# Kernel tuning notes

Hardware: AMD Instinct MI355X
Metric: run time of the kernel (lower is better)

Reference implementation:

```python
import jax, jax.numpy as jnp
import numpy as np

N_EMBED, D = 200000, 128
B, K = 50000, 32


def setup_inputs() -> dict:
    key = jax.random.key(0)
    k1, k2, k3 = jax.random.split(key, 3)
    embedding = jax.random.normal(k1, (N_EMBED, D), dtype=jnp.float32)
    self_feats = jax.random.normal(k2, (B, D), dtype=jnp.float32)
    neighbor_idx = jax.random.randint(k3, (B, K), 0, N_EMBED, dtype=jnp.int32)
    return {"embedding": embedding, "self_feats": self_feats, "neighbor_idx": neighbor_idx}


def reference(embedding, self_feats, neighbor_idx):
    # Original builds a row-normalized 0/1 mask over unique neighbors and does
    # mask @ embed_matrix == per-node mean of neighbor embeddings.
    neigh = jnp.take(embedding, neighbor_idx, axis=0)   # [B, K, D] gather
    feats_1 = jnp.mean(neigh, axis=1)                   # [B, D] segment-mean
    feats_2 = self_feats - feats_1                      # [B, D]
    return jnp.concatenate((feats_1, feats_2), axis=1)  # [B, 2D]
```

## Files before the change

### kernel.cpp

```cpp
#include <hip/hip_runtime.h>


constexpr int D = 128;
constexpr int K = 32;
constexpr int ROW_WORDS = D / 4;

typedef float f32x2 __attribute__((ext_vector_type(2)));

__global__ __launch_bounds__(256) void convert_f32_to_fp8(
    const float* __restrict__ in, unsigned int* __restrict__ out, int n16)
{
    int i = blockIdx.x * blockDim.x + threadIdx.x;
    if (i >= n16) return;
    const float4* p = reinterpret_cast<const float4*>(in) + (size_t)i * 4;
    float4 a = p[0], b = p[1], c = p[2], d = p[3];
    unsigned int w0 = 0, w1 = 0, w2 = 0, w3 = 0;
    w0 = __builtin_amdgcn_cvt_pk_fp8_f32(a.x, a.y, w0, false);
    w0 = __builtin_amdgcn_cvt_pk_fp8_f32(a.z, a.w, w0, true);
    w1 = __builtin_amdgcn_cvt_pk_fp8_f32(b.x, b.y, w1, false);
    w1 = __builtin_amdgcn_cvt_pk_fp8_f32(b.z, b.w, w1, true);
    w2 = __builtin_amdgcn_cvt_pk_fp8_f32(c.x, c.y, w2, false);
    w2 = __builtin_amdgcn_cvt_pk_fp8_f32(c.z, c.w, w2, true);
    w3 = __builtin_amdgcn_cvt_pk_fp8_f32(d.x, d.y, w3, false);
    w3 = __builtin_amdgcn_cvt_pk_fp8_f32(d.z, d.w, w3, true);
    uint4 pack; pack.x = w0; pack.y = w1; pack.z = w2; pack.w = w3;
    reinterpret_cast<uint4*>(out)[i] = pack;
}

__device__ __forceinline__ void acc_fp8x16(float* acc, const uint4& e)
{
    f32x2 t;
    t = __builtin_amdgcn_cvt_pk_f32_fp8(e.x, false); acc[0]  += t.x; acc[1]  += t.y;
    t = __builtin_amdgcn_cvt_pk_f32_fp8(e.x, true ); acc[2]  += t.x; acc[3]  += t.y;
    t = __builtin_amdgcn_cvt_pk_f32_fp8(e.y, false); acc[4]  += t.x; acc[5]  += t.y;
    t = __builtin_amdgcn_cvt_pk_f32_fp8(e.y, true ); acc[6]  += t.x; acc[7]  += t.y;
    t = __builtin_amdgcn_cvt_pk_f32_fp8(e.z, false); acc[8]  += t.x; acc[9]  += t.y;
    t = __builtin_amdgcn_cvt_pk_f32_fp8(e.z, true ); acc[10] += t.x; acc[11] += t.y;
    t = __builtin_amdgcn_cvt_pk_f32_fp8(e.w, false); acc[12] += t.x; acc[13] += t.y;
    t = __builtin_amdgcn_cvt_pk_f32_fp8(e.w, true ); acc[14] += t.x; acc[15] += t.y;
}

__global__ __launch_bounds__(256) void intra_agg_fp8(
    const unsigned int* __restrict__ emb,
    const float* __restrict__ self_feats,
    const int*   __restrict__ neighbor_idx,
    float*       __restrict__ out,
    int B)
{
    const int tid  = blockIdx.x * blockDim.x + threadIdx.x;
    const int row  = tid >> 3;
    const int lane = tid & 7;
    if (row >= B) return;

    const int* ip = neighbor_idx + (size_t)row * K;
    const int iA = ip[lane];
    const int iB = ip[lane + 8];
    const int iC = ip[lane + 16];
    const int iD = ip[lane + 24];
    const int cw = lane * 4;

    float acc[16];
    #pragma unroll
    for (int j = 0; j < 16; ++j) acc[j] = 0.f;

    #pragma unroll
    for (int k = 0; k < 8; ++k) {
        const int a = __shfl(iA, k, 8);
        const int b = __shfl(iB, k, 8);
        const int c = __shfl(iC, k, 8);
        const int d = __shfl(iD, k, 8);
        const uint4 ea = *reinterpret_cast<const uint4*>(emb + (size_t)a * ROW_WORDS + cw);
        const uint4 eb = *reinterpret_cast<const uint4*>(emb + (size_t)b * ROW_WORDS + cw);
        const uint4 ec = *reinterpret_cast<const uint4*>(emb + (size_t)c * ROW_WORDS + cw);
        const uint4 ed = *reinterpret_cast<const uint4*>(emb + (size_t)d * ROW_WORDS + cw);
        acc_fp8x16(acc, ea);
        acc_fp8x16(acc, eb);
        acc_fp8x16(acc, ec);
        acc_fp8x16(acc, ed);
    }

    const float inv = 1.0f / (float)K;
    const int c0 = lane * 16;
    const float4* sp = reinterpret_cast<const float4*>(self_feats + (size_t)row * D + c0);
    float* orow = out + (size_t)row * (2 * D);
    float4* om = reinterpret_cast<float4*>(orow + c0);
    float4* od = reinterpret_cast<float4*>(orow + D + c0);

    #pragma unroll
    for (int q = 0; q < 4; ++q) {
        float4 m;
        m.x = acc[4*q + 0] * inv;
        m.y = acc[4*q + 1] * inv;
        m.z = acc[4*q + 2] * inv;
        m.w = acc[4*q + 3] * inv;
        const float4 s = sp[q];
        float4 dd;
        dd.x = s.x - m.x; dd.y = s.y - m.y; dd.z = s.z - m.z; dd.w = s.w - m.w;
        om[q] = m;
        od[q] = dd;
    }
}

__global__ __launch_bounds__(256) void intra_agg_f32(
    const float* __restrict__ embedding,
    const float* __restrict__ self_feats,
    const int*   __restrict__ neighbor_idx,
    float*       __restrict__ out,
    int B)
{
    const int tid    = blockIdx.x * blockDim.x + threadIdx.x;
    const int row    = tid >> 5;
    const int lane32 = tid & 31;
    if (row >= B) return;

    const int my_idx = neighbor_idx[(size_t)row * K + lane32];
    const int c = lane32 * 4;

    float4 a0 = {0,0,0,0}, a1 = {0,0,0,0}, a2 = {0,0,0,0}, a3 = {0,0,0,0};
    #pragma unroll
    for (int k = 0; k < K; k += 4) {
        const int i0 = __shfl(my_idx, k + 0, 32);
        const int i1 = __shfl(my_idx, k + 1, 32);
        const int i2 = __shfl(my_idx, k + 2, 32);
        const int i3 = __shfl(my_idx, k + 3, 32);
        const float4 e0 = *reinterpret_cast<const float4*>(embedding + (size_t)i0 * D + c);
        const float4 e1 = *reinterpret_cast<const float4*>(embedding + (size_t)i1 * D + c);
        const float4 e2 = *reinterpret_cast<const float4*>(embedding + (size_t)i2 * D + c);
        const float4 e3 = *reinterpret_cast<const float4*>(embedding + (size_t)i3 * D + c);
        a0.x += e0.x; a0.y += e0.y; a0.z += e0.z; a0.w += e0.w;
        a1.x += e1.x; a1.y += e1.y; a1.z += e1.z; a1.w += e1.w;
        a2.x += e2.x; a2.y += e2.y; a2.z += e2.z; a2.w += e2.w;
        a3.x += e3.x; a3.y += e3.y; a3.z += e3.z; a3.w += e3.w;
    }

    const float inv = 1.0f / (float)K;
    float4 mean;
    mean.x = (a0.x + a1.x + a2.x + a3.x) * inv;
    mean.y = (a0.y + a1.y + a2.y + a3.y) * inv;
    mean.z = (a0.z + a1.z + a2.z + a3.z) * inv;
    mean.w = (a0.w + a1.w + a2.w + a3.w) * inv;

    const float4 self = *reinterpret_cast<const float4*>(self_feats + (size_t)row * D + c);
    float4 diff;
    diff.x = self.x - mean.x; diff.y = self.y - mean.y;
    diff.z = self.z - mean.z; diff.w = self.w - mean.w;

    float* orow = out + (size_t)row * (2 * D);
    *reinterpret_cast<float4*>(orow + c)     = mean;
    *reinterpret_cast<float4*>(orow + D + c) = diff;
}

extern "C" void kernel_launch(void* const* d_in, const int* in_sizes, int n_in,
                              void* d_out, int out_size, void* d_ws, size_t ws_size,
                              hipStream_t stream) {
    const float* embedding  = (const float*)d_in[0];
    const float* self_feats = (const float*)d_in[1];
    const int*   neigh_idx  = (const int*)d_in[2];
    float* out = (float*)d_out;

    const int n_embed_elems = in_sizes[0];
    const int B = in_sizes[1] / D;
    const size_t fp8_bytes = (size_t)n_embed_elems;

    if (ws_size >= fp8_bytes) {
        unsigned int* emb8 = (unsigned int*)d_ws;
        {
            const int n16 = n_embed_elems / 16;
            const int block = 256;
            const int grid = (n16 + block - 1) / block;
            convert_f32_to_fp8<<<grid, block, 0, stream>>>(embedding, emb8, n16);
        }
        {
            const long long total_threads = (long long)B * 8;
            const int block = 256;
            const int grid = (int)((total_threads + block - 1) / block);
            intra_agg_fp8<<<grid, block, 0, stream>>>(emb8, self_feats, neigh_idx, out, B);
        }
    } else {
        const long long total_threads = (long long)B * 32;
        const int block = 256;
        const int grid = (int)((total_threads + block - 1) / block);
        intra_agg_f32<<<grid, block, 0, stream>>>(embedding, self_feats, neigh_idx, out, B);
    }
}
```

Before: 217.5 us.

## Fuse fp8 conversion and aggregation into one cooperative persistent kernel

Replaces the two-launch path (convert to fp8, then gather-mean) with a single cooperative kernel. It runs a grid-stride conversion phase, calls grid.sync, then runs a grid-stride aggregation phase. Streaming loads and stores use nontemporal hints. The aim is to remove one launch gap and the associated tail idle time, at the cost of a grid-wide barrier and persistent-grid scheduling overhead. It falls back to the two-kernel path if cooperative launch is unavailable.

```diff
diff --git a/kernel.cpp b/kernel.cpp
--- a/kernel.cpp
+++ b/kernel.cpp
@@ -1,11 +1,116 @@
 #include <hip/hip_runtime.h>
+#include <hip/hip_cooperative_groups.h>
+
+namespace cg = cooperative_groups;
 
 
 constexpr int D = 128;
 constexpr int K = 32;
 constexpr int ROW_WORDS = D / 4;
 
-typedef float f32x2 __attribute__((ext_vector_type(2)));
+typedef float        f32x2  __attribute__((ext_vector_type(2)));
+typedef float        f32x4v __attribute__((ext_vector_type(4)));
+typedef unsigned int u32x4v __attribute__((ext_vector_type(4)));
+
+__device__ __forceinline__ void acc_fp8x16v(float* acc, const u32x4v e)
+{
+    f32x2 t;
+    t = __builtin_amdgcn_cvt_pk_f32_fp8(e[0], false); acc[0]  += t.x; acc[1]  += t.y;
+    t = __builtin_amdgcn_cvt_pk_f32_fp8(e[0], true ); acc[2]  += t.x; acc[3]  += t.y;
+    t = __builtin_amdgcn_cvt_pk_f32_fp8(e[1], false); acc[4]  += t.x; acc[5]  += t.y;
+    t = __builtin_amdgcn_cvt_pk_f32_fp8(e[1], true ); acc[6]  += t.x; acc[7]  += t.y;
+    t = __builtin_amdgcn_cvt_pk_f32_fp8(e[2], false); acc[8]  += t.x; acc[9]  += t.y;
+    t = __builtin_amdgcn_cvt_pk_f32_fp8(e[2], true ); acc[10] += t.x; acc[11] += t.y;
+    t = __builtin_amdgcn_cvt_pk_f32_fp8(e[3], false); acc[12] += t.x; acc[13] += t.y;
+    t = __builtin_amdgcn_cvt_pk_f32_fp8(e[3], true ); acc[14] += t.x; acc[15] += t.y;
+}
+
+__global__ __launch_bounds__(256, 4) void fused_intra_agg(
+    const float* __restrict__ emb_f32,
+    unsigned int* __restrict__ emb8,
+    const float* __restrict__ self_feats,
+    const int*   __restrict__ neighbor_idx,
+    float*       __restrict__ out,
+    int n16, int B)
+{
+    cg::grid_group grid = cg::this_grid();
+    const int gtid = blockIdx.x * blockDim.x + threadIdx.x;
+    const int gsz  = gridDim.x * blockDim.x;
+
+    for (int i = gtid; i < n16; i += gsz) {
+        const f32x4v* p = reinterpret_cast<const f32x4v*>(emb_f32) + (size_t)i * 4;
+        const f32x4v a = __builtin_nontemporal_load(p);
+        const f32x4v b = __builtin_nontemporal_load(p + 1);
+        const f32x4v c = __builtin_nontemporal_load(p + 2);
+        const f32x4v d = __builtin_nontemporal_load(p + 3);
+        unsigned int w0 = 0, w1 = 0, w2 = 0, w3 = 0;
+        w0 = __builtin_amdgcn_cvt_pk_fp8_f32(a[0], a[1], w0, false);
+        w0 = __builtin_amdgcn_cvt_pk_fp8_f32(a[2], a[3], w0, true);
+        w1 = __builtin_amdgcn_cvt_pk_fp8_f32(b[0], b[1], w1, false);
+        w1 = __builtin_amdgcn_cvt_pk_fp8_f32(b[2], b[3], w1, true);
+        w2 = __builtin_amdgcn_cvt_pk_fp8_f32(c[0], c[1], w2, false);
+        w2 = __builtin_amdgcn_cvt_pk_fp8_f32(c[2], c[3], w2, true);
+        w3 = __builtin_amdgcn_cvt_pk_fp8_f32(d[0], d[1], w3, false);
+        w3 = __builtin_amdgcn_cvt_pk_fp8_f32(d[2], d[3], w3, true);
+        u32x4v pack; pack[0] = w0; pack[1] = w1; pack[2] = w2; pack[3] = w3;
+        reinterpret_cast<u32x4v*>(emb8)[i] = pack;
+    }
+
+    grid.sync();
+
+    const int   nwork = B * 8;
+    const float inv   = 1.0f / (float)K;
+    for (int t = gtid; t < nwork; t += gsz) {
+        const int row  = t >> 3;
+        const int lane = t & 7;
+
+        const int* ip = neighbor_idx + (size_t)row * K;
+        const int iA = __builtin_nontemporal_load(ip + lane);
+        const int iB = __builtin_nontemporal_load(ip + lane + 8);
+        const int iC = __builtin_nontemporal_load(ip + lane + 16);
+        const int iD = __builtin_nontemporal_load(ip + lane + 24);
+        const int cw = lane * 4;
+
+        float acc[16];
+        #pragma unroll
+        for (int j = 0; j < 16; ++j) acc[j] = 0.f;
+
+        #pragma unroll
+        for (int k = 0; k < 8; ++k) {
+            const int a = __shfl(iA, k, 8);
+            const int b = __shfl(iB, k, 8);
+            const int c = __shfl(iC, k, 8);
+            const int d = __shfl(iD, k, 8);
+            const u32x4v ea = *reinterpret_cast<const u32x4v*>(emb8 + (size_t)a * ROW_WORDS + cw);
+            const u32x4v eb = *reinterpret_cast<const u32x4v*>(emb8 + (size_t)b * ROW_WORDS + cw);
+            const u32x4v ec = *reinterpret_cast<const u32x4v*>(emb8 + (size_t)c * ROW_WORDS + cw);
+            const u32x4v ed = *reinterpret_cast<const u32x4v*>(emb8 + (size_t)d * ROW_WORDS + cw);
+            acc_fp8x16v(acc, ea);
+            acc_fp8x16v(acc, eb);
+            acc_fp8x16v(acc, ec);
+            acc_fp8x16v(acc, ed);
+        }
+
+        const int c0 = lane * 16;
+        const f32x4v* sp = reinterpret_cast<const f32x4v*>(self_feats + (size_t)row * D + c0);
+        float* orow = out + (size_t)row * (2 * D);
+        f32x4v* om = reinterpret_cast<f32x4v*>(orow + c0);
+        f32x4v* od = reinterpret_cast<f32x4v*>(orow + D + c0);
+
+        #pragma unroll
+        for (int q = 0; q < 4; ++q) {
+            f32x4v m;
+            m[0] = acc[4*q + 0] * inv;
+            m[1] = acc[4*q + 1] * inv;
+            m[2] = acc[4*q + 2] * inv;
+            m[3] = acc[4*q + 3] * inv;
+            const f32x4v s = __builtin_nontemporal_load(sp + q);
+            const f32x4v dd = s - m;
+            __builtin_nontemporal_store(m,  om + q);
+            __builtin_nontemporal_store(dd, od + q);
+        }
+    }
+}
 
 __global__ __launch_bounds__(256) void convert_f32_to_fp8(
     const float* __restrict__ in, unsigned int* __restrict__ out, int n16)
@@ -27,19 +132,6 @@
     reinterpret_cast<uint4*>(out)[i] = pack;
 }
 
-__device__ __forceinline__ void acc_fp8x16(float* acc, const uint4& e)
-{
-    f32x2 t;
-    t = __builtin_amdgcn_cvt_pk_f32_fp8(e.x, false); acc[0]  += t.x; acc[1]  += t.y;
-    t = __builtin_amdgcn_cvt_pk_f32_fp8(e.x, true ); acc[2]  += t.x; acc[3]  += t.y;
-    t = __builtin_amdgcn_cvt_pk_f32_fp8(e.y, false); acc[4]  += t.x; acc[5]  += t.y;
-    t = __builtin_amdgcn_cvt_pk_f32_fp8(e.y, true ); acc[6]  += t.x; acc[7]  += t.y;
-    t = __builtin_amdgcn_cvt_pk_f32_fp8(e.z, false); acc[8]  += t.x; acc[9]  += t.y;
-    t = __builtin_amdgcn_cvt_pk_f32_fp8(e.z, true ); acc[10] += t.x; acc[11] += t.y;
-    t = __builtin_amdgcn_cvt_pk_f32_fp8(e.w, false); acc[12] += t.x; acc[13] += t.y;
-    t = __builtin_amdgcn_cvt_pk_f32_fp8(e.w, true ); acc[14] += t.x; acc[15] += t.y;
-}
-
 __global__ __launch_bounds__(256) void intra_agg_fp8(
     const unsigned int* __restrict__ emb,
     const float* __restrict__ self_feats,
@@ -69,14 +161,14 @@
         const int b = __shfl(iB, k, 8);
         const int c = __shfl(iC, k, 8);
         const int d = __shfl(iD, k, 8);
-        const uint4 ea = *reinterpret_cast<const uint4*>(emb + (size_t)a * ROW_WORDS + cw);
-        const uint4 eb = *reinterpret_cast<const uint4*>(emb + (size_t)b * ROW_WORDS + cw);
-        const uint4 ec = *reinterpret_cast<const uint4*>(emb + (size_t)c * ROW_WORDS + cw);
-        const uint4 ed = *reinterpret_cast<const uint4*>(emb + (size_t)d * ROW_WORDS + cw);
-        acc_fp8x16(acc, ea);
-        acc_fp8x16(acc, eb);
-        acc_fp8x16(acc, ec);
-        acc_fp8x16(acc, ed);
+        const u32x4v ea = *reinterpret_cast<const u32x4v*>(emb + (size_t)a * ROW_WORDS + cw);
+        const u32x4v eb = *reinterpret_cast<const u32x4v*>(emb + (size_t)b * ROW_WORDS + cw);
+        const u32x4v ec = *reinterpret_cast<const u32x4v*>(emb + (size_t)c * ROW_WORDS + cw);
+        const u32x4v ed = *reinterpret_cast<const u32x4v*>(emb + (size_t)d * ROW_WORDS + cw);
+        acc_fp8x16v(acc, ea);
+        acc_fp8x16v(acc, eb);
+        acc_fp8x16v(acc, ec);
+        acc_fp8x16v(acc, ed);
     }
 
     const float inv = 1.0f / (float)K;
@@ -152,7 +244,8 @@
 
 extern "C" void kernel_launch(void* const* d_in, const int* in_sizes, int n_in,
                               void* d_out, int out_size, void* d_ws, size_t ws_size,
-                              hipStream_t stream) {
+                              hipStream_t stream)
+{
     const float* embedding  = (const float*)d_in[0];
     const float* self_feats = (const float*)d_in[1];
     const int*   neigh_idx  = (const int*)d_in[2];
@@ -161,20 +254,49 @@
     const int n_embed_elems = in_sizes[0];
     const int B = in_sizes[1] / D;
     const size_t fp8_bytes = (size_t)n_embed_elems;
+    const int n16 = n_embed_elems / 16;
 
     if (ws_size >= fp8_bytes) {
         unsigned int* emb8 = (unsigned int*)d_ws;
-        {
-            const int n16 = n_embed_elems / 16;
+
+        static int coop_state = -1;
+        static int nblk = 0;
+        if (coop_state < 0) {
+            int dev = 0;
+            (void)hipGetDevice(&dev);
+            int attr = 0;
+            (void)hipDeviceGetAttribute(&attr, hipDeviceAttributeCooperativeLaunch, dev);
+            hipDeviceProp_t prop{};
+            (void)hipGetDeviceProperties(&prop, dev);
+            int bpm = 0;
+            (void)hipOccupancyMaxActiveBlocksPerMultiprocessor(&bpm, fused_intra_agg, 256, 0);
+            long long nb = (long long)bpm * (long long)prop.multiProcessorCount;
+            if (nb > 2048) nb = 2048;
+            nblk = (int)nb;
+            coop_state = (attr != 0 && nblk >= 128) ? 1 : 0;
+        }
+
+        bool launched = false;
+        if (coop_state == 1) {
+            int n16v = n16, Bv = B;
+            void* args[] = { (void*)&embedding, (void*)&emb8, (void*)&self_feats,
+                             (void*)&neigh_idx, (void*)&out, (void*)&n16v, (void*)&Bv };
+            hipError_t e = hipLaunchCooperativeKernel(fused_intra_agg, dim3(nblk),
+                                                      dim3(256), args, 0, stream);
+            if (e == hipSuccess) {
+                launched = true;
+            } else {
+                (void)hipGetLastError();
+                coop_state = 0;
+            }
+        }
+        if (!launched) {
             const int block = 256;
-            const int grid = (n16 + block - 1) / block;
-            convert_f32_to_fp8<<<grid, block, 0, stream>>>(embedding, emb8, n16);
-        }
-        {
+            const int grid1 = (n16 + block - 1) / block;
+            convert_f32_to_fp8<<<grid1, block, 0, stream>>>(embedding, emb8, n16);
             const long long total_threads = (long long)B * 8;
-            const int block = 256;
-            const int grid = (int)((total_threads + block - 1) / block);
-            intra_agg_fp8<<<grid, block, 0, stream>>>(emb8, self_feats, neigh_idx, out, B);
+            const int grid2 = (int)((total_threads + block - 1) / block);
+            intra_agg_fp8<<<grid2, block, 0, stream>>>(emb8, self_feats, neigh_idx, out, B);
         }
     } else {
         const long long total_threads = (long long)B * 32;
```

After: 444.9 us. 2.05x slower.
